# Optimization experiments

Measured on AMD Instinct MI355X. Metric: run time of the kernel, lower is better.

The kernel has to match this reference:

```python
import jax, jax.numpy as jnp
import numpy as np

N, M, FEAT, POS, D, MSG, NCLS = 64, 32, 256, 6, 262, 128, 7


def setup_inputs() -> dict:
    key = jax.random.key(0)
    ks = jax.random.split(key, 12)
    s = 0.05
    p = lambda k, shape: jax.random.normal(k, shape, jnp.float32) * s
    return {
        "nodes_feature": jax.random.normal(ks[0], (N, M, FEAT), jnp.float32),
        "pos": jax.random.normal(ks[1], (N, M, POS), jnp.float32),
        "num_rec": jax.random.randint(ks[2], (N,), 1, M + 1),
        "link_w1": p(ks[3], (D, 2 * D)),
        "link_b1": jnp.zeros((D,), jnp.float32),
        "link_w2": p(ks[4], (D,)),
        "link_b2": jnp.zeros((), jnp.float32),
        "msg_w": p(ks[5], (MSG, D)),
        "msg_b": jnp.zeros((MSG,), jnp.float32),
        "gru_w_ih": p(ks[6], (3 * D, MSG)),
        "gru_w_hh": p(ks[7], (3 * D, D)),
        "gru_b_ih": jnp.zeros((3 * D,), jnp.float32),
        "gru_b_hh": jnp.zeros((3 * D,), jnp.float32),
        "ro_w1": p(ks[8], (MSG, D)),
        "ro_b1": jnp.zeros((MSG,), jnp.float32),
        "ro_w2": p(ks[9], (NCLS, MSG)),
        "ro_b2": jnp.zeros((NCLS,), jnp.float32),
    }


def reference(nodes_feature, pos, num_rec, link_w1, link_b1, link_w2, link_b2,
              msg_w, msg_b, gru_w_ih, gru_w_hh, gru_b_ih, gru_b_hh,
              ro_w1, ro_b1, ro_w2, ro_b2):
    # node_feat = [resnet_feat, pos]  -> (N, M, 262)
    nf = jnp.concatenate([nodes_feature, pos], axis=-1)
    n, m, d = nf.shape
    valid = jnp.arange(m)[None, :] < num_rec[:, None]          # (N, M)
    pair = valid[:, :, None] & valid[:, None, :]               # (N, M, M)

    # edge_feat[b,:,i,j] = concat(nf[b,i], nf[b,j]); zero for invalid pairs
    ef = jnp.concatenate([
        jnp.broadcast_to(nf[:, :, None, :], (n, m, m, d)),
        jnp.broadcast_to(nf[:, None, :, :], (n, m, m, d)),
    ], axis=-1) * pair[..., None].astype(nf.dtype)             # (N, M, M, 2D)

    # 1x1 convs == per-pair MLP
    hlink = jax.nn.relu(jnp.einsum('bnwc,dc->bnwd', ef, link_w1) + link_b1)
    attmat = jax.nn.sigmoid(jnp.einsum('bnwd,d->bnw', hlink, link_w2) + link_b2)

    # messages are only summed over valid sender nodes w
    att_m = attmat * valid[:, None, :].astype(attmat.dtype)    # (N, M, M)

    def gru_step(x, h):
        # PyTorch GRU cell: gates order (r, z, n)
        gx = x @ gru_w_ih.T + gru_b_ih
        gh = h @ gru_w_hh.T + gru_b_hh
        xr, xz, xn = jnp.split(gx, 3, axis=-1)
        hr, hz, hn = jnp.split(gh, 3, axis=-1)
        r = jax.nn.sigmoid(xr + hr)
        z = jax.nn.sigmoid(xz + hz)
        c = jnp.tanh(xn + r * hn)
        return (1.0 - z) * c + z * h

    vmask = valid[..., None].astype(nf.dtype)
    h_state = nf                                               # pass 0 input state
    for _ in range(2):                                         # two message-passing rounds
        msg = h_state @ msg_w.T + msg_b                        # (N, M, 128)
        m_v = jnp.einsum('bnw,bwk->bnk', att_m, msg)           # attention-weighted sum
        h_state = gru_step(m_v, h_state) * vmask               # invalid nodes stay zero

    pred = (jax.nn.relu(h_state @ ro_w1.T + ro_b1) @ ro_w2.T + ro_b2) * vmask
    return pred, attmat
```

## Files before the change

kernel.cpp:

```cpp
#include <hip/hip_runtime.h>
#include <math.h>

#define N_G   64
#define M_N   32
#define FEAT  256
#define POSD  6
#define D     262
#define MSG   128
#define NCLS  7

#define KA_S  424
#define KHW   288
#define KFULL 416
#define PSTR  320

#define S_PROJ (528*288)
#define S_MSG  (128*288)
#define S_RZ   (544*416)
#define S_XN   (272*128)
#define S_HN   (272*288)
#define S_RO   (128*288)
#define S_RO2  (16*128)

#define O_WPROJ 0u
#define O_WMSG  76032u
#define O_WRZ   94464u
#define O_WXN   207616u
#define O_WHN   225024u
#define O_WRO   264192u
#define O_WRO2  282624u
#define O_GB    283648u

typedef __attribute__((ext_vector_type(8))) short short8;
typedef __attribute__((ext_vector_type(4))) short short4v;
typedef __attribute__((ext_vector_type(4))) float floatx4;

#define MFMA __builtin_amdgcn_mfma_f32_16x16x32_bf16

__device__ __forceinline__ short f2bf(float f) {
    union { float f; unsigned u; } v; v.f = f;
    unsigned r = v.u + 0x7FFF + ((v.u >> 16) & 1);
    return (short)(r >> 16);
}
__device__ __forceinline__ float bf2f(short s) {
    union { float f; unsigned u; } v;
    v.u = ((unsigned)(unsigned short)s) << 16;
    return v.f;
}
__device__ __forceinline__ float sigf(float x) {
    return __builtin_amdgcn_rcpf(1.f + __expf(-x));
}
__device__ __forceinline__ float tanh_fast(float x) {
    float e = __expf(-2.f * fabsf(x));
    float t = (1.f - e) * __builtin_amdgcn_rcpf(1.f + e);
    return copysignf(t, x);
}

__global__ void prep_kernel(const float* __restrict__ w1, const float* __restrict__ msg_w,
                            const float* __restrict__ w_ih, const float* __restrict__ w_hh,
                            const float* __restrict__ ro_w1, const float* __restrict__ ro_w2,
                            const float* __restrict__ b_ih, const float* __restrict__ b_hh,
                            float* __restrict__ ws)
{
    short* wproj = (short*)(ws + O_WPROJ);
    short* wmsg  = (short*)(ws + O_WMSG);
    short* wrz   = (short*)(ws + O_WRZ);
    short* wxn   = (short*)(ws + O_WXN);
    short* whn   = (short*)(ws + O_WHN);
    short* wro   = (short*)(ws + O_WRO);
    short* wro2  = (short*)(ws + O_WRO2);
    float* gb    = ws + O_GB;
    const int TOT_S = S_PROJ + S_MSG + S_RZ + S_XN + S_HN + S_RO + S_RO2;
    const int TOTAL = TOT_S + 1088;
    for (int i = blockIdx.x * blockDim.x + threadIdx.x; i < TOTAL;
         i += gridDim.x * blockDim.x) {
        int idx = i;
        if (idx < S_PROJ) {
            int n = idx / 288, k = idx % 288;
            float v = 0.f;
            if (k < D && n < 524)
                v = (n < D) ? w1[n * 524 + k] : w1[(n - D) * 524 + D + k];
            wproj[idx] = f2bf(v);
            continue;
        }
        idx -= S_PROJ;
        if (idx < S_MSG) {
            int n = idx / 288, k = idx % 288;
            wmsg[idx] = f2bf(k < D ? msg_w[n * D + k] : 0.f);
            continue;
        }
        idx -= S_MSG;
        if (idx < S_RZ) {
            int g = idx / 416, k = idx % 416;
            int gi = (g < 272) ? 0 : 1;
            int d = g - gi * 272;
            float v = 0.f;
            if (d < D) {
                int row = gi * D + d;
                if (k < 128)            v = w_ih[row * MSG + k];
                else if (k < 128 + D)   v = w_hh[row * D + (k - 128)];
            }
            wrz[idx] = f2bf(v);
            continue;
        }
        idx -= S_RZ;
        if (idx < S_XN) {
            int d = idx / 128, k = idx % 128;
            wxn[idx] = f2bf(d < D ? w_ih[(2 * D + d) * MSG + k] : 0.f);
            continue;
        }
        idx -= S_XN;
        if (idx < S_HN) {
            int d = idx / 288, k = idx % 288;
            whn[idx] = f2bf((d < D && k < D) ? w_hh[(2 * D + d) * D + k] : 0.f);
            continue;
        }
        idx -= S_HN;
        if (idx < S_RO) {
            int n = idx / 288, k = idx % 288;
            wro[idx] = f2bf(k < D ? ro_w1[n * D + k] : 0.f);
            continue;
        }
        idx -= S_RO;
        if (idx < S_RO2) {
            int n = idx / 128, k = idx % 128;
            wro2[idx] = f2bf(n < NCLS ? ro_w2[n * MSG + k] : 0.f);
            continue;
        }
        idx -= S_RO2;
        {
            int seg = idx / 272, d = idx % 272;
            float v = 0.f;
            if (d < D) {
                if (seg == 0)      v = b_ih[d] + b_hh[d];
                else if (seg == 1) v = b_ih[D + d] + b_hh[D + d];
                else if (seg == 2) v = b_ih[2 * D + d];
                else               v = b_hh[2 * D + d];
            }
            gb[idx] = v;
        }
    }
}

__global__ __launch_bounds__(1024) void fused_kernel(
    const float* __restrict__ nodes, const float* __restrict__ pos,
    const int* __restrict__ nrec_g,
    const float* __restrict__ b1g, const float* __restrict__ w2g,
    const float* __restrict__ b2g, const float* __restrict__ msg_bg,
    const float* __restrict__ ro_b1g, const float* __restrict__ ro_b2g,
    const float* __restrict__ ws,
    float* __restrict__ att_out, float* __restrict__ pred)
{
    const short* Wproj = (const short*)(ws + O_WPROJ);
    const short* Wmsg  = (const short*)(ws + O_WMSG);
    const short* Wrz   = (const short*)(ws + O_WRZ);
    const short* Wxn   = (const short*)(ws + O_WXN);
    const short* Whn   = (const short*)(ws + O_WHN);
    const short* Wro   = (const short*)(ws + O_WRO);
    const short* Wro2  = (const short*)(ws + O_WRO2);
    const float* gb    = ws + O_GB;

    __shared__ __align__(16) short bufA[32 * KA_S];
    __shared__ __align__(16) short bufB[32 * KA_S];
    __shared__ __align__(16) short paL[32 * PSTR];
    __shared__ __align__(16) short pbL[32 * PSTR];
    __shared__ __align__(16) short attL[32 * 40];
    __shared__ __align__(16) short msgT[128 * 40];
    __shared__ __align__(16) short hidL[32 * 136];
    __shared__ __align__(16) float b1L[PSTR], w2L[PSTR];

    const int b = blockIdx.x;
    const int tid = threadIdx.x;
    const int wave = tid >> 6, lane = tid & 63;
    const int quad = lane >> 4, lrow = lane & 15;
    const int nr = nrec_g[b];

    for (int idx = tid; idx < 32 * 64; idx += 1024) {
        int w = idx >> 6, c4 = idx & 63;
        floatx4 v = *(const floatx4*)(nodes + ((size_t)(b * 32 + w)) * FEAT + c4 * 4);
        short4v s; s[0] = f2bf(v[0]); s[1] = f2bf(v[1]); s[2] = f2bf(v[2]); s[3] = f2bf(v[3]);
        *(short4v*)(bufA + w * KA_S + 128 + c4 * 4) = s;
    }
    for (int idx = tid; idx < 32 * POSD; idx += 1024) {
        int w = idx / POSD, c = idx % POSD;
        bufA[w * KA_S + 128 + FEAT + c] = f2bf(pos[((size_t)(b * 32 + w)) * POSD + c]);
    }
    for (int idx = tid; idx < 32 * 34; idx += 1024) {
        int w = idx / 34, c = idx % 34;
        bufA[w * KA_S + 390 + c] = 0;
        bufB[w * KA_S + 390 + c] = 0;
    }
    for (int idx = tid; idx < 32 * (PSTR - D); idx += 1024) {
        int w = idx / (PSTR - D), c = idx % (PSTR - D);
        paL[w * PSTR + D + c] = 0;
        pbL[w * PSTR + D + c] = 0;
    }
    for (int d = tid; d < PSTR; d += 1024) {
        b1L[d] = (d < D) ? b1g[d] : 0.f;
        w2L[d] = (d < D) ? w2g[d] : 0.f;
    }
    __syncthreads();

    for (int s = wave; s < 41; s += 16) {
        floatx4 acc0 = {}, acc1 = {};
        const short* bw = (s < 33)
            ? Wproj + (s * 16 + lrow) * KHW + quad * 8
            : Wmsg + ((s - 33) * 16 + lrow) * KHW + quad * 8;
        const short* ap = bufA + lrow * KA_S + 128 + quad * 8;
        for (int kk = 0; kk < 9; ++kk) {
            short8 a0 = *(const short8*)(ap + kk * 32);
            short8 a1 = *(const short8*)(ap + 16 * KA_S + kk * 32);
            short8 bv = *(const short8*)(bw + kk * 32);
            acc0 = MFMA(a0, bv, acc0, 0, 0, 0);
            acc1 = MFMA(a1, bv, acc1, 0, 0, 0);
        }
        if (s < 33) {
            int col = s * 16 + lrow;
#pragma unroll
            for (int rr = 0; rr < 4; ++rr) {
                int r0 = quad * 4 + rr;
                if (col < D) {
                    paL[r0 * PSTR + col] = f2bf(acc0[rr]);
                    paL[(r0 + 16) * PSTR + col] = f2bf(acc1[rr]);
                } else if (col < 2 * D) {
                    pbL[r0 * PSTR + (col - D)] = f2bf(acc0[rr]);
                    pbL[(r0 + 16) * PSTR + (col - D)] = f2bf(acc1[rr]);
                }
            }
        } else {
            int col = (s - 33) * 16 + lrow;
            float bias = msg_bg[col];
#pragma unroll
            for (int rr = 0; rr < 4; ++rr) {
                msgT[col * 40 + quad * 4 + rr] = f2bf(acc0[rr] + bias);
                msgT[col * 40 + 16 + quad * 4 + rr] = f2bf(acc1[rr] + bias);
            }
        }
    }
    __syncthreads();

    {
        const int grp = tid >> 4;
        const int i   = grp >> 1;
        const int jh  = (grp & 1) * 16;
        const int c16 = tid & 15;
        const float b2v = b2g[0];
        float pav[5][4], b1v[5][4], w2v[5][4];
#pragma unroll
        for (int k = 0; k < 5; ++k) {
            int dbase = c16 * 4 + 64 * k;
            short4v p = *(const short4v*)(paL + i * PSTR + dbase);
            floatx4 bb = *(const floatx4*)(b1L + dbase);
            floatx4 ww = *(const floatx4*)(w2L + dbase);
#pragma unroll
            for (int e = 0; e < 4; ++e) {
                pav[k][e] = bf2f(p[e]); b1v[k][e] = bb[e]; w2v[k][e] = ww[e];
            }
        }
        float p0 = 0.f;
#pragma unroll
        for (int k = 0; k < 5; ++k)
#pragma unroll
            for (int e = 0; e < 4; ++e)
                p0 += fmaxf(b1v[k][e], 0.f) * w2v[k][e];
        p0 += __shfl_down(p0, 8, 16); p0 += __shfl_down(p0, 4, 16);
        p0 += __shfl_down(p0, 2, 16); p0 += __shfl_down(p0, 1, 16);
        float c0 = sigf(p0 + b2v);
        const bool vi = i < nr;
        for (int jj = 0; jj < 16; ++jj) {
            int j = jh + jj;
            float a;
            if (j < nr && vi) {
                const short* pb = pbL + j * PSTR + c16 * 4;
                float s = 0.f;
#pragma unroll
                for (int k = 0; k < 5; ++k) {
                    short4v q = *(const short4v*)(pb + 64 * k);
#pragma unroll
                    for (int e = 0; e < 4; ++e) {
                        float v = pav[k][e] + bf2f(q[e]) + b1v[k][e];
                        s += fmaxf(v, 0.f) * w2v[k][e];
                    }
                }
                s += __shfl_down(s, 8, 16); s += __shfl_down(s, 4, 16);
                s += __shfl_down(s, 2, 16); s += __shfl_down(s, 1, 16);
                a = sigf(s + b2v);
            } else {
                a = c0;
            }
            if (c16 == 0) {
                att_out[((size_t)(b * 32 + i)) * 32 + j] = a;
                attL[i * 40 + j] = f2bf((j < nr) ? a : 0.f);
            }
        }
    }
    __syncthreads();

    for (int rnd = 0; rnd < 2; ++rnd) {
        short* src = rnd ? bufB : bufA;
        short* dst = rnd ? bufA : bufB;

        if (rnd) {
            int s = wave >> 1, mi = wave & 1;
            floatx4 acc = {};
            const short* bw = Wmsg + (s * 16 + lrow) * KHW + quad * 8;
            const short* ap = src + (mi * 16 + lrow) * KA_S + 128 + quad * 8;
            for (int kk = 0; kk < 9; ++kk) {
                short8 a0 = *(const short8*)(ap + kk * 32);
                short8 bv = *(const short8*)(bw + kk * 32);
                acc = MFMA(a0, bv, acc, 0, 0, 0);
            }
            int col = s * 16 + lrow;
            float bias = msg_bg[col];
#pragma unroll
            for (int rr = 0; rr < 4; ++rr)
                msgT[col * 40 + mi * 16 + quad * 4 + rr] = f2bf(acc[rr] + bias);
            __syncthreads();
        }

        {
            int mi = wave & 1, ng = wave >> 1;
            short8 afrag = *(const short8*)(attL + (mi * 16 + lrow) * 40 + quad * 8);
            floatx4 acc = {};
            short8 bf0 = *(const short8*)(msgT + (ng * 16 + lrow) * 40 + quad * 8);
            acc = MFMA(afrag, bf0, acc, 0, 0, 0);
#pragma unroll
            for (int rr = 0; rr < 4; ++rr) {
                int m = mi * 16 + quad * 4 + rr;
                src[m * KA_S + ng * 16 + lrow] = f2bf(acc[rr]);
            }
        }
        __syncthreads();

        for (int u = wave; u < 34; u += 16) {
            int s = u >> 1, half = u & 1;
            floatx4 aR = {}, aZ = {}, aN = {}, aH = {};
            const short* ap  = src + (half * 16 + lrow) * KA_S + quad * 8;
            const short* bpr = Wrz + (s * 16 + lrow) * KFULL + quad * 8;
            const short* bpz = Wrz + (272 + s * 16 + lrow) * KFULL + quad * 8;
            const short* bpx = Wxn + (s * 16 + lrow) * 128 + quad * 8;
            const short* bph = Whn + (s * 16 + lrow) * KHW + quad * 8;
            for (int kk = 0; kk < 13; ++kk) {
                short8 a0 = *(const short8*)(ap + kk * 32);
                short8 br = *(const short8*)(bpr + kk * 32);
                short8 bz = *(const short8*)(bpz + kk * 32);
                aR = MFMA(a0, br, aR, 0, 0, 0);
                aZ = MFMA(a0, bz, aZ, 0, 0, 0);
                if (kk < 4) {
                    short8 bx = *(const short8*)(bpx + kk * 32);
                    aN = MFMA(a0, bx, aN, 0, 0, 0);
                } else {
                    short8 bh = *(const short8*)(bph + (kk - 4) * 32);
                    aH = MFMA(a0, bh, aH, 0, 0, 0);
                }
            }
            int d = s * 16 + lrow;
            if (d < D) {
                float bgr = gb[d], bgz = gb[272 + d];
                float bxv = gb[544 + d], bhv = gb[816 + d];
#pragma unroll
                for (int rr = 0; rr < 4; ++rr) {
                    int m = half * 16 + quad * 4 + rr;
                    float rg = sigf(aR[rr] + bgr);
                    float zg = sigf(aZ[rr] + bgz);
                    float cg = tanh_fast(aN[rr] + bxv + rg * (aH[rr] + bhv));
                    float hold = bf2f(src[m * KA_S + 128 + d]);
                    float hv = (1.f - zg) * cg + zg * hold;
                    if (m >= nr) hv = 0.f;
                    dst[m * KA_S + 128 + d] = f2bf(hv);
                }
            }
        }
        __syncthreads();
    }

    {
        int s = wave >> 1, mi = wave & 1;
        floatx4 acc = {};
        const short* bw = Wro + (s * 16 + lrow) * KHW + quad * 8;
        const short* ap = bufA + (mi * 16 + lrow) * KA_S + 128 + quad * 8;
        for (int kk = 0; kk < 9; ++kk) {
            short8 a0 = *(const short8*)(ap + kk * 32);
            short8 bv = *(const short8*)(bw + kk * 32);
            acc = MFMA(a0, bv, acc, 0, 0, 0);
        }
        int col = s * 16 + lrow;
        float bias = ro_b1g[col];
#pragma unroll
        for (int rr = 0; rr < 4; ++rr)
            hidL[(mi * 16 + quad * 4 + rr) * 136 + col] = f2bf(fmaxf(acc[rr] + bias, 0.f));
    }
    __syncthreads();

    if (wave < 2) {
        floatx4 acc = {};
        const short* ap = hidL + (wave * 16 + lrow) * 136 + quad * 8;
        const short* bw = Wro2 + lrow * 128 + quad * 8;
        for (int kk = 0; kk < 4; ++kk) {
            short8 a0 = *(const short8*)(ap + kk * 32);
            short8 bv = *(const short8*)(bw + kk * 32);
            acc = MFMA(a0, bv, acc, 0, 0, 0);
        }
        int q = lrow;
        if (q < NCLS) {
            float bias = ro_b2g[q];
#pragma unroll
            for (int rr = 0; rr < 4; ++rr) {
                int m = wave * 16 + quad * 4 + rr;
                float v = acc[rr] + bias;
                if (m >= nr) v = 0.f;
                pred[((size_t)(b * 32 + m)) * NCLS + q] = v;
            }
        }
    }
}

extern "C" void kernel_launch(void* const* d_in, const int* in_sizes, int n_in,
                              void* d_out, int out_size, void* d_ws, size_t ws_size,
                              hipStream_t stream)
{
    const float* nodes = (const float*)d_in[0];
    const float* pos   = (const float*)d_in[1];
    const int*   nrec  = (const int*)d_in[2];
    const float* w1    = (const float*)d_in[3];
    const float* b1    = (const float*)d_in[4];
    const float* w2    = (const float*)d_in[5];
    const float* b2    = (const float*)d_in[6];
    const float* msg_w = (const float*)d_in[7];
    const float* msg_b = (const float*)d_in[8];
    const float* w_ih  = (const float*)d_in[9];
    const float* w_hh  = (const float*)d_in[10];
    const float* b_ih  = (const float*)d_in[11];
    const float* b_hh  = (const float*)d_in[12];
    const float* ro_w1 = (const float*)d_in[13];
    const float* ro_b1 = (const float*)d_in[14];
    const float* ro_w2 = (const float*)d_in[15];
    const float* ro_b2 = (const float*)d_in[16];
    float* ws   = (float*)d_ws;
    float* pred = (float*)d_out;
    float* attout = pred + (size_t)N_G * M_N * NCLS;

    prep_kernel<<<256, 256, 0, stream>>>(w1, msg_w, w_ih, w_hh, ro_w1, ro_w2,
                                         b_ih, b_hh, ws);
    fused_kernel<<<N_G, 1024, 0, stream>>>(nodes, pos, nrec, b1, w2, b2, msg_b,
                                           ro_b1, ro_b2, ws, attout, pred);
}
```

Before: 162.1 us.

## Prefetch MFMA weight fragments into registers ahead of compute across all GEMM stages

New measurement: 176.4 us. 8.9% more time.

```diff
diff --git a/kernel.cpp b/kernel.cpp
--- a/kernel.cpp
+++ b/kernel.cpp
@@ -175,6 +175,13 @@
     const int quad = lane >> 4, lrow = lane & 15;
     const int nr = nrec_g[b];
 
+    short8 wv0[9];
+    {
+        const short* bw = Wproj + (wave * 16 + lrow) * KHW + quad * 8;
+#pragma unroll
+        for (int kk = 0; kk < 9; ++kk) wv0[kk] = *(const short8*)(bw + kk * 32);
+    }
+
     for (int idx = tid; idx < 32 * 64; idx += 1024) {
         int w = idx >> 6, c4 = idx & 63;
         floatx4 v = *(const floatx4*)(nodes + ((size_t)(b * 32 + w)) * FEAT + c4 * 4);
@@ -201,20 +208,18 @@
     }
     __syncthreads();
 
-    for (int s = wave; s < 41; s += 16) {
-        floatx4 acc0 = {}, acc1 = {};
-        const short* bw = (s < 33)
-            ? Wproj + (s * 16 + lrow) * KHW + quad * 8
-            : Wmsg + ((s - 33) * 16 + lrow) * KHW + quad * 8;
-        const short* ap = bufA + lrow * KA_S + 128 + quad * 8;
-        for (int kk = 0; kk < 9; ++kk) {
-            short8 a0 = *(const short8*)(ap + kk * 32);
-            short8 a1 = *(const short8*)(ap + 16 * KA_S + kk * 32);
-            short8 bv = *(const short8*)(bw + kk * 32);
-            acc0 = MFMA(a0, bv, acc0, 0, 0, 0);
-            acc1 = MFMA(a1, bv, acc1, 0, 0, 0);
-        }
-        if (s < 33) {
+    {
+        auto compute_tile = [&](const short8* wv, floatx4& acc0, floatx4& acc1) {
+            const short* ap = bufA + lrow * KA_S + 128 + quad * 8;
+#pragma unroll
+            for (int kk = 0; kk < 9; ++kk) {
+                short8 a0 = *(const short8*)(ap + kk * 32);
+                short8 a1 = *(const short8*)(ap + 16 * KA_S + kk * 32);
+                acc0 = MFMA(a0, wv[kk], acc0, 0, 0, 0);
+                acc1 = MFMA(a1, wv[kk], acc1, 0, 0, 0);
+            }
+        };
+        auto store_proj = [&](int s, const floatx4& acc0, const floatx4& acc1) {
             int col = s * 16 + lrow;
 #pragma unroll
             for (int rr = 0; rr < 4; ++rr) {
@@ -227,7 +232,8 @@
                     pbL[(r0 + 16) * PSTR + (col - D)] = f2bf(acc1[rr]);
                 }
             }
-        } else {
+        };
+        auto store_msg = [&](int s, const floatx4& acc0, const floatx4& acc1) {
             int col = (s - 33) * 16 + lrow;
             float bias = msg_bg[col];
 #pragma unroll
@@ -235,6 +241,38 @@
                 msgT[col * 40 + quad * 4 + rr] = f2bf(acc0[rr] + bias);
                 msgT[col * 40 + 16 + quad * 4 + rr] = f2bf(acc1[rr] + bias);
             }
+        };
+
+        const int t1 = wave + 16;
+        short8 wv1[9];
+        {
+            const short* bw = Wproj + (t1 * 16 + lrow) * KHW + quad * 8;
+#pragma unroll
+            for (int kk = 0; kk < 9; ++kk) wv1[kk] = *(const short8*)(bw + kk * 32);
+        }
+        floatx4 a0 = {}, a1 = {};
+        compute_tile(wv0, a0, a1);
+
+        const int t2 = wave + 32;
+        const bool has2 = t2 < 41;
+        if (has2) {
+            const short* bw = (t2 < 33)
+                ? Wproj + (t2 * 16 + lrow) * KHW + quad * 8
+                : Wmsg + ((t2 - 33) * 16 + lrow) * KHW + quad * 8;
+#pragma unroll
+            for (int kk = 0; kk < 9; ++kk) wv0[kk] = *(const short8*)(bw + kk * 32);
+        }
+        store_proj(wave, a0, a1);
+
+        floatx4 b0 = {}, b1 = {};
+        compute_tile(wv1, b0, b1);
+        store_proj(t1, b0, b1);
+
+        if (has2) {
+            floatx4 c0 = {}, c1 = {};
+            compute_tile(wv0, c0, c1);
+            if (t2 < 33) store_proj(t2, c0, c1);
+            else         store_msg(t2, c0, c1);
         }
     }
     __syncthreads();
@@ -302,13 +340,16 @@
 
         if (rnd) {
             int s = wave >> 1, mi = wave & 1;
+            const short* bw = Wmsg + (s * 16 + lrow) * KHW + quad * 8;
+            short8 wm[9];
+#pragma unroll
+            for (int kk = 0; kk < 9; ++kk) wm[kk] = *(const short8*)(bw + kk * 32);
             floatx4 acc = {};
-            const short* bw = Wmsg + (s * 16 + lrow) * KHW + quad * 8;
             const short* ap = src + (mi * 16 + lrow) * KA_S + 128 + quad * 8;
+#pragma unroll
             for (int kk = 0; kk < 9; ++kk) {
                 short8 a0 = *(const short8*)(ap + kk * 32);
-                short8 bv = *(const short8*)(bw + kk * 32);
-                acc = MFMA(a0, bv, acc, 0, 0, 0);
+                acc = MFMA(a0, wm[kk], acc, 0, 0, 0);
             }
             int col = s * 16 + lrow;
             float bias = msg_bg[col];
@@ -334,26 +375,38 @@
 
         for (int u = wave; u < 34; u += 16) {
             int s = u >> 1, half = u & 1;
-            floatx4 aR = {}, aZ = {}, aN = {}, aH = {};
             const short* ap  = src + (half * 16 + lrow) * KA_S + quad * 8;
             const short* bpr = Wrz + (s * 16 + lrow) * KFULL + quad * 8;
-            const short* bpz = Wrz + (272 + s * 16 + lrow) * KFULL + quad * 8;
+            const short* bpz = bpr + 272 * KFULL;
             const short* bpx = Wxn + (s * 16 + lrow) * 128 + quad * 8;
             const short* bph = Whn + (s * 16 + lrow) * KHW + quad * 8;
+
+            short8 wr[13], wx[4];
+#pragma unroll
+            for (int kk = 0; kk < 13; ++kk) wr[kk] = *(const short8*)(bpr + kk * 32);
+#pragma unroll
+            for (int kk = 0; kk < 4; ++kk)  wx[kk] = *(const short8*)(bpx + kk * 32);
+
+            floatx4 aR = {}, aZ = {}, aN = {}, aH = {};
+#pragma unroll
             for (int kk = 0; kk < 13; ++kk) {
                 short8 a0 = *(const short8*)(ap + kk * 32);
-                short8 br = *(const short8*)(bpr + kk * 32);
-                short8 bz = *(const short8*)(bpz + kk * 32);
-                aR = MFMA(a0, br, aR, 0, 0, 0);
-                aZ = MFMA(a0, bz, aZ, 0, 0, 0);
-                if (kk < 4) {
-                    short8 bx = *(const short8*)(bpx + kk * 32);
-                    aN = MFMA(a0, bx, aN, 0, 0, 0);
-                } else {
-                    short8 bh = *(const short8*)(bph + (kk - 4) * 32);
-                    aH = MFMA(a0, bh, aH, 0, 0, 0);
-                }
-            }
+                aR = MFMA(a0, wr[kk], aR, 0, 0, 0);
+                if (kk < 4) aN = MFMA(a0, wx[kk], aN, 0, 0, 0);
+                wr[kk] = *(const short8*)(bpz + kk * 32);
+            }
+#pragma unroll
+            for (int kk = 0; kk < 13; ++kk) {
+                short8 a0 = *(const short8*)(ap + kk * 32);
+                aZ = MFMA(a0, wr[kk], aZ, 0, 0, 0);
+                if (kk < 9) wr[kk] = *(const short8*)(bph + kk * 32);
+            }
+#pragma unroll
+            for (int kk = 0; kk < 9; ++kk) {
+                short8 a0 = *(const short8*)(ap + (4 + kk) * 32);
+                aH = MFMA(a0, wr[kk], aH, 0, 0, 0);
+            }
+
             int d = s * 16 + lrow;
             if (d < D) {
                 float bgr = gb[d], bgz = gb[272 + d];
@@ -376,13 +429,16 @@
 
     {
         int s = wave >> 1, mi = wave & 1;
+        const short* bw = Wro + (s * 16 + lrow) * KHW + quad * 8;
+        short8 wv[9];
+#pragma unroll
+        for (int kk = 0; kk < 9; ++kk) wv[kk] = *(const short8*)(bw + kk * 32);
         floatx4 acc = {};
-        const short* bw = Wro + (s * 16 + lrow) * KHW + quad * 8;
         const short* ap = bufA + (mi * 16 + lrow) * KA_S + 128 + quad * 8;
+#pragma unroll
         for (int kk = 0; kk < 9; ++kk) {
             short8 a0 = *(const short8*)(ap + kk * 32);
-            short8 bv = *(const short8*)(bw + kk * 32);
-            acc = MFMA(a0, bv, acc, 0, 0, 0);
+            acc = MFMA(a0, wv[kk], acc, 0, 0, 0);
         }
         int col = s * 16 + lrow;
         float bias = ro_b1g[col];
@@ -393,13 +449,16 @@
     __syncthreads();
 
     if (wave < 2) {
+        const short* bw = Wro2 + lrow * 128 + quad * 8;
+        short8 wv[4];
+#pragma unroll
+        for (int kk = 0; kk < 4; ++kk) wv[kk] = *(const short8*)(bw + kk * 32);
         floatx4 acc = {};
         const short* ap = hidL + (wave * 16 + lrow) * 136 + quad * 8;
-        const short* bw = Wro2 + lrow * 128 + quad * 8;
+#pragma unroll
         for (int kk = 0; kk < 4; ++kk) {
             short8 a0 = *(const short8*)(ap + kk * 32);
-            short8 bv = *(const short8*)(bw + kk * 32);
-            acc = MFMA(a0, bv, acc, 0, 0, 0);
+            acc = MFMA(a0, wv[kk], acc, 0, 0, 0);
         }
         int q = lrow;
         if (q < NCLS) {
```
